# Kernel optimization log

Hardware: AMD Instinct MI355X
Metric: run time of the kernel (lower is better)

Reference implementation:

```python
import jax, jax.numpy as jnp
import numpy as np

B, C, H, W = 4, 64, 256, 256
P, PRIOR, HID, HEADS, NPROMPT = 4, 64, 128, 4, 4
TOKEN = C * P * P  # 1024
RATIO = 0.25


def _patchify(x):
    b, c, h, w = x.shape
    gh, gw = h // P, w // P
    t = x.reshape(b, c, gh, P, gw, P).transpose(0, 2, 4, 1, 3, 5).reshape(b, gh * gw, c * P * P)
    return t, (b, c, gh, gw)


def _unpatchify(t, meta):
    b, c, gh, gw = meta
    return t.reshape(b, gh, gw, c, P, P).transpose(0, 3, 1, 4, 2, 5).reshape(b, c, gh * P, gw * P)


def _coords(gh, gw):
    ys = (jnp.arange(gh, dtype=jnp.float32) + 0.5) / gh
    xs = (jnp.arange(gw, dtype=jnp.float32) + 0.5) / gw
    yy, xx = jnp.meshgrid(ys, xs, indexing='ij')
    return jnp.stack([yy.ravel(), xx.ravel()], axis=-1)  # [N, 2]


def setup_inputs():
    key = jax.random.key(0)
    ks = iter(jax.random.split(key, 32))
    rn = lambda *s: jax.random.normal(next(ks), s, jnp.float32)
    w = lambda *s: rn(*s) * 0.02
    z = lambda *s: jnp.zeros(s, jnp.float32)
    return dict(
        vis_feat=rn(B, C, H, W),
        ir_feat=rn(B, C, H, W),
        prompt_bank=w(NPROMPT, PRIOR),
        Wr=w(2 * C, NPROMPT), br=z(NPROMPT),
        br_Wtok=w(2, 2 * TOKEN, HID), br_Wpri=w(2, PRIOR, HID), br_Wco=w(2, 2, HID),
        br_bs=z(2, HID), br_Wout=w(2, HID), br_bout=z(2),
        br_Wq=w(2, TOKEN, HID), br_Wk=w(2, TOKEN, HID), br_Wv=w(2, TOKEN, HID),
        br_Wo=w(2, HID, TOKEN), br_Wint=w(2, PRIOR, HID),
        br_Wbyp=w(2, 2 * TOKEN, TOKEN), br_bbyp=z(2, TOKEN),
        conv1_w=w(C, C, 3, 3), conv1_b=z(C),
        conv2_w=w(C, C, 3, 3), conv2_b=z(C),
        Wa1=w(PRIOR, 2 * C), ba1=z(2 * C),
        Wa2=w(2 * C, 2 * C), ba2=z(2 * C),
    )


def reference(vis_feat, ir_feat, prompt_bank, Wr, br, br_Wtok, br_Wpri, br_Wco, br_bs, br_Wout, br_bout, br_Wq, br_Wk, br_Wv, br_Wo, br_Wint, br_Wbyp, br_bbyp, conv1_w, conv1_b, conv2_w, conv2_b, Wa1, ba1, Wa2, ba2):
    # intent router: pooled features -> prompt mixture -> intent vector
    pooled = jnp.concatenate([vis_feat.mean((2, 3)), ir_feat.mean((2, 3))], -1)  # [B, 2C]
    prompt_weight = jax.nn.softmax(pooled @ Wr + br, -1)  # [B, NPROMPT]
    intent = prompt_weight @ prompt_bank  # [B, PRIOR]

    def split(x):
        F = jnp.fft.fft2(x)
        return jnp.abs(F), jnp.angle(F)

    vamp, vph = split(vis_feat)
    iamp, iph = split(ir_feat)

    def fuse(vm, im, i):
        vt, meta = _patchify(vm)
        it_, _ = _patchify(im)
        b, c, gh, gw = meta
        n = gh * gw
        coords = _coords(gh, gw)
        # token score net: tokens + intent + coord embedding -> scalar score per token
        h = (jnp.concatenate([vt, it_], -1) @ br_Wtok[i]
             + (intent @ br_Wpri[i])[:, None, :]
             + (coords @ br_Wco[i])[None] + br_bs[i])
        score = jax.nn.gelu(h) @ br_Wout[i] + br_bout[i]  # [B, N]
        k = max(1, int(n * RATIO))
        topk_val, topk_idx = jax.lax.top_k(score, k)
        gth = lambda t: jnp.take_along_axis(t, topk_idx[:, :, None], axis=1)
        vs, irs = gth(vt), gth(it_)  # [B, k, TOKEN]
        # selected-token cross attention (vis queries, ir keys/values), intent-modulated
        dh = HID // HEADS
        hd = lambda x, Wm: (x @ Wm).reshape(b, k, HEADS, dh)
        q, kk, vv = hd(vs, br_Wq[i]), hd(irs, br_Wk[i]), hd(irs, br_Wv[i])
        attn = jax.nn.softmax(jnp.einsum('bqhd,bkhd->bhqk', q, kk) / jnp.float32(np.sqrt(dh)), -1)
        o = jnp.einsum('bhqk,bkhd->bqhd', attn, vv).reshape(b, k, HID)
        o = o + (intent @ br_Wint[i])[:, None, :]
        fused_sel = vs + o @ br_Wo[i]  # [B, k, TOKEN]
        # lightweight bypass on all tokens (gated blend), then scatter selected back
        g = jax.nn.sigmoid(jnp.concatenate([vt, it_], -1) @ br_Wbyp[i] + br_bbyp[i])
        full = g * vt + (1.0 - g) * it_
        full = full.at[jnp.arange(b)[:, None], topk_idx].set(fused_sel)
        return _unpatchify(full, meta)

    famp = fuse(vamp, iamp, 0)
    fph = fuse(vph, iph, 1)
    fph = jnp.arctan2(jnp.sin(fph), jnp.cos(fph))  # phase wrap to (-pi, pi]
    spec = jax.lax.complex(famp * jnp.cos(fph), famp * jnp.sin(fph))
    spatial = jnp.fft.ifft2(spec).real

    conv = lambda x, wgt, bia: jax.lax.conv_general_dilated(
        x, wgt, (1, 1), 'SAME', dimension_numbers=('NCHW', 'OIHW', 'NCHW')) + bia[None, :, None, None]
    y = conv(jax.nn.relu(conv(spatial, conv1_w, conv1_b)), conv2_w, conv2_b)
    aff = jax.nn.gelu(intent @ Wa1 + ba1) @ Wa2 + ba2  # [B, 2C]
    gamma, beta = aff[:, :C], aff[:, C:]
    y = y * (1.0 + 0.1 * jnp.tanh(gamma))[:, :, None, None] + 0.1 * beta[:, :, None, None]
    return y + 0.5 * (vis_feat + ir_feat)
```

## Files before the change

kernel.cpp:

```cpp
#include <hip/hip_runtime.h>

typedef unsigned int uint;
typedef unsigned short ushort;
typedef unsigned long long u64;
typedef __attribute__((ext_vector_type(8))) short short8;
typedef __attribute__((ext_vector_type(4))) float f32x4;

__device__ __forceinline__ uint brev8(uint x){ return __brev(x) >> 24; }
__device__ __forceinline__ float geluf(float x){
  return 0.5f*x*(1.f + tanhf(0.7978845608028654f*(x + 0.044715f*x*x*x)));
}
__device__ __forceinline__ ushort f2bf(float f){
  unsigned u = __float_as_uint(f);
  unsigned r = u + 0x7FFFu + ((u >> 16) & 1u);
  return (ushort)(r >> 16);
}
__device__ __forceinline__ float bf2f(ushort u){
  return __uint_as_float((uint)u << 16);
}

__global__ __launch_bounds__(256) void kern_pool(const float* __restrict__ vis,
                                                 const float* __restrict__ irf,
                                                 float* __restrict__ pooled){
  __shared__ float red[256];
  int bc = blockIdx.x;
  int b = bc >> 7, cc = bc & 127;
  const float* src = (cc < 64) ? (vis + (size_t)(b*64+cc)*65536)
                               : (irf + (size_t)(b*64+(cc-64))*65536);
  float s = 0.f;
  for (int i = threadIdx.x; i < 65536; i += 256) s += src[i];
  red[threadIdx.x] = s;
  __syncthreads();
  for (int off = 128; off > 0; off >>= 1){
    if (threadIdx.x < off) red[threadIdx.x] += red[threadIdx.x + off];
    __syncthreads();
  }
  if (threadIdx.x == 0) pooled[bc] = red[0] * (1.f/65536.f);
}

__global__ __launch_bounds__(256) void kern_small(const float* __restrict__ pooled,
    const float* __restrict__ Wr, const float* __restrict__ br,
    const float* __restrict__ bank, const float* __restrict__ Wpri,
    const float* __restrict__ Wint, const float* __restrict__ Wa1,
    const float* __restrict__ ba1, const float* __restrict__ Wa2,
    const float* __restrict__ ba2,
    float* __restrict__ IP, float* __restrict__ IPint,
    float* __restrict__ modg, float* __restrict__ modb){
  __shared__ float logit_s[16];
  __shared__ float pw_s[16];
  __shared__ float intent_s[4][64];
  __shared__ float t1_s[4][128];
  int t = threadIdx.x;
  if (t < 16){
    int b = t >> 2, j = t & 3;
    float s = br[j];
    for (int k = 0; k < 128; ++k) s += pooled[b*128+k]*Wr[k*4+j];
    logit_s[t] = s;
  }
  __syncthreads();
  if (t < 4){
    int b = t;
    float m = logit_s[b*4];
    for (int j = 1; j < 4; ++j) m = fmaxf(m, logit_s[b*4+j]);
    float e[4], sum = 0.f;
    for (int j = 0; j < 4; ++j){ e[j] = expf(logit_s[b*4+j]-m); sum += e[j]; }
    for (int j = 0; j < 4; ++j) pw_s[b*4+j] = e[j]/sum;
  }
  __syncthreads();
  {
    int b = t >> 6, p = t & 63;
    float s = 0.f;
    for (int j = 0; j < 4; ++j) s += pw_s[b*4+j]*bank[j*64+p];
    intent_s[b][p] = s;
  }
  __syncthreads();
  for (int o = t; o < 1024; o += 256){
    int i = o >> 9, rem = o & 511, b = rem >> 7, n = rem & 127;
    float s1 = 0.f, s2 = 0.f;
    for (int p = 0; p < 64; ++p){
      float iv = intent_s[b][p];
      s1 += iv * Wpri[(i*64+p)*128 + n];
      s2 += iv * Wint[(i*64+p)*128 + n];
    }
    IP[o] = s1; IPint[o] = s2;
  }
  for (int o = t; o < 512; o += 256){
    int b = o >> 7, n = o & 127;
    float s = ba1[n];
    for (int p = 0; p < 64; ++p) s += intent_s[b][p]*Wa1[p*128+n];
    t1_s[b][n] = geluf(s);
  }
  __syncthreads();
  for (int o = t; o < 512; o += 256){
    int b = o >> 7, n = o & 127;
    float s = ba2[n];
    for (int p = 0; p < 128; ++p) s += t1_s[b][p]*Wa2[p*128+n];
    if (n < 64) modg[b*64+n] = 1.f + 0.1f*tanhf(s);
    else        modb[b*64+(n-64)] = 0.1f*s;
  }
}

__global__ __launch_bounds__(256) void kern_fft_rows_fwd(const float* __restrict__ x,
    float* __restrict__ sre, float* __restrict__ sim){
  __shared__ float re[2][256], im[2][256];
  __shared__ float twr[128], twi[128];
  int t = threadIdx.x;
  if (t < 128){
    float a = -6.2831853071795864f * (float)t * (1.f/256.f);
    sincosf(a, &twi[t], &twr[t]);
  }
  int r = t >> 7, jj = t & 127;
  size_t row = (size_t)blockIdx.x*2 + r;
  {
    const float* xp = x + row*256;
    re[r][jj] = xp[jj]; re[r][jj+128] = xp[jj+128];
    im[r][jj] = 0.f;    im[r][jj+128] = 0.f;
  }
  __syncthreads();
  for (int s = 0; s < 8; ++s){
    int half = 128 >> s;
    int j = jj & (half-1);
    int g = jj >> (7-s);
    int k = (g << (8-s)) + j;
    int m = j << s;
    float wc = twr[m], ws = twi[m];
    float are = re[r][k],      aim = im[r][k];
    float bre = re[r][k+half], bim = im[r][k+half];
    re[r][k] = are + bre; im[r][k] = aim + bim;
    float tr = are - bre, ti = aim - bim;
    re[r][k+half] = tr*wc - ti*ws;
    im[r][k+half] = tr*ws + ti*wc;
    __syncthreads();
  }
  {
    float* orp = sre + row*256; float* oip = sim + row*256;
    int w1 = jj, w2 = jj + 128;
    orp[w1] = re[r][brev8(w1)]; oip[w1] = im[r][brev8(w1)];
    orp[w2] = re[r][brev8(w2)]; oip[w2] = im[r][brev8(w2)];
  }
}

__global__ __launch_bounds__(256) void kern_ifft_rows_spec(const float* __restrict__ famp,
    const float* __restrict__ fph, float* __restrict__ sre, float* __restrict__ sim){
  __shared__ float re[4][256], im[4][256];
  __shared__ float twr[128], twi[128];
  int t = threadIdx.x;
  if (t < 128){
    float a = -6.2831853071795864f * (float)t * (1.f/256.f);
    sincosf(a, &twi[t], &twr[t]);
  }
  int R = blockIdx.x * 4;
  {
    int r = t >> 6, q = t & 63;
    int row = R + r;
    int bc = row >> 8, h = row & 255;
    int b = bc >> 6, c = bc & 63;
    size_t addr = ((size_t)(b*4096 + (h>>2)*64 + q))*1024 + c*16 + (h&3)*4;
    float4 a4 = *(const float4*)(famp + addr);
    float4 p4 = *(const float4*)(fph + addr);
    float sn, cs;
    sincosf(p4.x, &sn, &cs); re[r][4*q+0] = a4.x*cs; im[r][4*q+0] = a4.x*sn;
    sincosf(p4.y, &sn, &cs); re[r][4*q+1] = a4.y*cs; im[r][4*q+1] = a4.y*sn;
    sincosf(p4.z, &sn, &cs); re[r][4*q+2] = a4.z*cs; im[r][4*q+2] = a4.z*sn;
    sincosf(p4.w, &sn, &cs); re[r][4*q+3] = a4.w*cs; im[r][4*q+3] = a4.w*sn;
  }
  __syncthreads();
  for (int s = 0; s < 8; ++s){
    int half = 128 >> s;
    #pragma unroll
    for (int bi0 = 0; bi0 < 2; ++bi0){
      int bi = t + bi0*256;
      int r = bi >> 7, tj = bi & 127;
      int j = tj & (half-1);
      int g = tj >> (7-s);
      int k = (g << (8-s)) + j;
      int m = j << s;
      float wc = twr[m], ws = -twi[m];
      float are = re[r][k],      aim = im[r][k];
      float bre = re[r][k+half], bim = im[r][k+half];
      re[r][k] = are + bre; im[r][k] = aim + bim;
      float tr = are - bre, ti = aim - bim;
      re[r][k+half] = tr*wc - ti*ws;
      im[r][k+half] = tr*ws + ti*wc;
    }
    __syncthreads();
  }
  {
    int r = t >> 6, q = t & 63;
    size_t row = (size_t)R + r;
    float4 vr, vi;
    vr.x = re[r][brev8(4*q+0)]; vi.x = im[r][brev8(4*q+0)];
    vr.y = re[r][brev8(4*q+1)]; vi.y = im[r][brev8(4*q+1)];
    vr.z = re[r][brev8(4*q+2)]; vi.z = im[r][brev8(4*q+2)];
    vr.w = re[r][brev8(4*q+3)]; vi.w = im[r][brev8(4*q+3)];
    *(float4*)(sre + row*256 + 4*q) = vr;
    *(float4*)(sim + row*256 + 4*q) = vi;
  }
}

template<int DIR>
__global__ __launch_bounds__(256) void kern_fft_cols(const float* __restrict__ sre,
    const float* __restrict__ sim, void* __restrict__ out0, void* __restrict__ out1){
  __shared__ float reL[256*17];
  __shared__ float imL[256*17];
  __shared__ float twr[128], twi[128];
  int t = threadIdx.x;
  if (t < 128){
    float a = -6.2831853071795864f * (float)t * (1.f/256.f);
    sincosf(a, &twi[t], &twr[t]);
  }
  int img = blockIdx.x >> 4;
  int c0 = (blockIdx.x & 15) * 16;
  {
    const float* pr = sre + ((size_t)img*256 + t)*256 + c0;
    const float* pi = sim + ((size_t)img*256 + t)*256 + c0;
    #pragma unroll
    for (int p = 0; p < 4; ++p){
      float4 vr = *(const float4*)(pr + 4*p);
      float4 vi = *(const float4*)(pi + 4*p);
      int base = t*17 + 4*p;
      reL[base+0]=vr.x; reL[base+1]=vr.y; reL[base+2]=vr.z; reL[base+3]=vr.w;
      imL[base+0]=vi.x; imL[base+1]=vi.y; imL[base+2]=vi.z; imL[base+3]=vi.w;
    }
  }
  __syncthreads();
  int col = t & 15, tb = t >> 4;
  for (int s = 0; s < 8; ++s){
    int half = 128 >> s;
    #pragma unroll
    for (int it = 0; it < 8; ++it){
      int tj = tb + it*16;
      int j = tj & (half-1);
      int g = tj >> (7-s);
      int k = (g << (8-s)) + j;
      int m = j << s;
      float wc = twr[m];
      float ws = (DIR == 0) ? twi[m] : -twi[m];
      int i0 = k*17 + col, i1 = (k+half)*17 + col;
      float are = reL[i0], aim = imL[i0];
      float bre = reL[i1], bim = imL[i1];
      reL[i0] = are + bre; imL[i0] = aim + bim;
      float tr = are - bre, ti = aim - bim;
      reL[i1] = tr*wc - ti*ws;
      imL[i1] = tr*ws + ti*wc;
    }
    __syncthreads();
  }
  int b = img >> 6, c = img & 63;
  int h = t; int src = (int)brev8((uint)h);
  if (DIR == 0){
    ushort* oa = (ushort*)out0;
    ushort* op = (ushort*)out1;
    int gy = h >> 2, py = h & 3;
    #pragma unroll
    for (int p = 0; p < 4; ++p){
      int base = src*17 + 4*p;
      float a0, a1, a2, a3, p0, p1, p2, p3;
      float rr, ii;
      rr = reL[base+0]; ii = imL[base+0]; a0 = sqrtf(rr*rr+ii*ii); p0 = atan2f(ii, rr);
      rr = reL[base+1]; ii = imL[base+1]; a1 = sqrtf(rr*rr+ii*ii); p1 = atan2f(ii, rr);
      rr = reL[base+2]; ii = imL[base+2]; a2 = sqrtf(rr*rr+ii*ii); p2 = atan2f(ii, rr);
      rr = reL[base+3]; ii = imL[base+3]; a3 = sqrtf(rr*rr+ii*ii); p3 = atan2f(ii, rr);
      size_t addr = ((size_t)(b*4096 + gy*64 + (c0>>2) + p))*1024 + c*16 + py*4;
      uint2 av, pv;
      av.x = (uint)f2bf(a0) | ((uint)f2bf(a1) << 16);
      av.y = (uint)f2bf(a2) | ((uint)f2bf(a3) << 16);
      pv.x = (uint)f2bf(p0) | ((uint)f2bf(p1) << 16);
      pv.y = (uint)f2bf(p2) | ((uint)f2bf(p3) << 16);
      *(uint2*)(oa + addr) = av;
      *(uint2*)(op + addr) = pv;
    }
  } else {
    float* op = (float*)out0 + ((size_t)img*256 + h)*256 + c0;
    #pragma unroll
    for (int p = 0; p < 4; ++p){
      int base = src*17 + 4*p;
      float4 v;
      v.x = reL[base+0]*(1.f/65536.f);
      v.y = reL[base+1]*(1.f/65536.f);
      v.z = reL[base+2]*(1.f/65536.f);
      v.w = reL[base+3]*(1.f/65536.f);
      *(float4*)(op + 4*p) = v;
    }
  }
}

struct TRS {
  const float* src[10];
  ushort* dst[10];
  int K[10], N[10];
  int start[11];
};
__global__ __launch_bounds__(256) void kern_tr(TRS p){
  __shared__ float lds[32][33];
  int bid = blockIdx.x;
  int e = 0;
  while (bid >= p.start[e+1]) ++e;
  int tloc = bid - p.start[e];
  int tilesN = p.N[e] >> 5;
  int tn = tloc % tilesN, tk = tloc / tilesN;
  int k0 = tk << 5, n0 = tn << 5;
  const float* src = p.src[e];
  ushort* dst = p.dst[e];
  int K = p.K[e], N = p.N[e];
  int r = threadIdx.x >> 5, c = threadIdx.x & 31;
  #pragma unroll
  for (int i = 0; i < 4; ++i)
    lds[r + 8*i][c] = src[(size_t)(k0 + r + 8*i)*N + n0 + c];
  __syncthreads();
  #pragma unroll
  for (int i = 0; i < 4; ++i)
    dst[(size_t)(n0 + r + 8*i)*K + k0 + c] = f2bf(lds[c][r + 8*i]);
}

struct GP2 {
  const ushort* A0[6];
  const ushort* Bt[6];
  float* Cm[6];
  const int* idxp[6];
  int N, K;
};

__global__ __launch_bounds__(256) void kern_mgemm2(GP2 p){
  __shared__ __align__(16) ushort Asb[64*64];
  __shared__ __align__(16) ushort Bsb[128*64];
  __shared__ int idx_s[64];
  int z = blockIdx.z;
  const ushort* A0 = p.A0[z];
  const ushort* Bt = p.Bt[z];
  float* Cm = p.Cm[z];
  int tid = threadIdx.x;
  int m0 = blockIdx.x * 64;
  int n0 = blockIdx.y * 128;
  int lane = tid & 63, w = tid >> 6;
  int wr = w & 1, wc = w >> 1;
  int lr = lane & 15, ql = lane >> 4;

  if (tid < 64){
    int m = m0 + tid;
    idx_s[tid] = p.idxp[z][(m >> 10)*1024 + (m & 1023)];
  }
  __syncthreads();
  int gb = m0 >> 10;

  f32x4 acc[2][4];
  #pragma unroll
  for (int i = 0; i < 2; ++i)
    #pragma unroll
    for (int j = 0; j < 4; ++j) acc[i][j] = (f32x4){0.f,0.f,0.f,0.f};

  int kh = tid & 7;
  int rA = tid >> 3;
  for (int k0 = 0; k0 < p.K; k0 += 64){
    #pragma unroll
    for (int s = 0; s < 2; ++s){
      int m = rA + 32*s;
      const ushort* ap = A0 + ((size_t)(gb << 12) + idx_s[m])*(size_t)p.K + k0 + kh*8;
      short8 v = *(const short8*)ap;
      int byte = m*128 + ((kh*16) ^ ((m & 7)*16));
      *(short8*)((char*)Asb + byte) = v;
    }
    #pragma unroll
    for (int s = 0; s < 4; ++s){
      int n = rA + 32*s;
      short8 v = *(const short8*)(Bt + (size_t)(n0+n)*p.K + k0 + kh*8);
      int byte = n*128 + ((kh*16) ^ ((n & 7)*16));
      *(short8*)((char*)Bsb + byte) = v;
    }
    __syncthreads();
    short8 af[2][2], bf[4][2];
    #pragma unroll
    for (int fm = 0; fm < 2; ++fm){
      int row = wr*32 + fm*16 + lr;
      #pragma unroll
      for (int kq = 0; kq < 2; ++kq){
        int byte = row*128 + ((kq*64 + ql*16) ^ ((row & 7)*16));
        af[fm][kq] = *(const short8*)((const char*)Asb + byte);
      }
    }
    #pragma unroll
    for (int fn = 0; fn < 4; ++fn){
      int row = wc*64 + fn*16 + lr;
      #pragma unroll
      for (int kq = 0; kq < 2; ++kq){
        int byte = row*128 + ((kq*64 + ql*16) ^ ((row & 7)*16));
        bf[fn][kq] = *(const short8*)((const char*)Bsb + byte);
      }
    }
    #pragma unroll
    for (int kq = 0; kq < 2; ++kq)
      #pragma unroll
      for (int fm = 0; fm < 2; ++fm)
        #pragma unroll
        for (int fn = 0; fn < 4; ++fn)
          acc[fm][fn] = __builtin_amdgcn_mfma_f32_16x16x32_bf16(af[fm][kq], bf[fn][kq],
                                                                acc[fm][fn], 0, 0, 0);
    __syncthreads();
  }

  #pragma unroll
  for (int fm = 0; fm < 2; ++fm){
    #pragma unroll
    for (int fn = 0; fn < 4; ++fn){
      int n = n0 + wc*64 + fn*16 + lr;
      #pragma unroll
      for (int reg = 0; reg < 4; ++reg){
        int m = m0 + wr*32 + fm*16 + ql*4 + reg;
        Cm[(size_t)m*p.N + n] = acc[fm][fn][reg];
      }
    }
  }
}

struct GP3 {
  const ushort* A0[2];
  const ushort* A1[2];
  const ushort* Bt[2];
  float* Ch[2];
  float* Cm[2];
  const float* ep0[2];
  const float* ep1[2];
  const float* ep2[2];
  const float* bias[2];
  const ushort* vt[2];
  const ushort* it[2];
  int K;
};

__global__ __launch_bounds__(256) void kern_mgemm3(GP3 p){
  __shared__ __align__(16) ushort Asb[128*64];
  __shared__ __align__(16) ushort Bsb[128*64];
  int z = blockIdx.z;
  const ushort* Bt = p.Bt[z];
  int tid = threadIdx.x;
  int m0 = blockIdx.x * 128;
  int n0 = blockIdx.y * 128;
  int lane = tid & 63, w = tid >> 6;
  int wr = w & 1, wc = w >> 1;
  int lr = lane & 15, ql = lane >> 4;

  f32x4 acc[4][4];
  #pragma unroll
  for (int i = 0; i < 4; ++i)
    #pragma unroll
    for (int j = 0; j < 4; ++j) acc[i][j] = (f32x4){0.f,0.f,0.f,0.f};

  int kh = tid & 7;
  int rA = tid >> 3;
  for (int k0 = 0; k0 < p.K; k0 += 64){
    const ushort* Asrc = (k0 < 1024) ? p.A0[z] : p.A1[z];
    int kk = (k0 & 1023) + kh*8;
    #pragma unroll
    for (int s = 0; s < 4; ++s){
      int m = rA + 32*s;
      short8 v = *(const short8*)(Asrc + (size_t)(m0+m)*1024 + kk);
      int byte = m*128 + ((kh*16) ^ ((m & 7)*16));
      *(short8*)((char*)Asb + byte) = v;
    }
    #pragma unroll
    for (int s = 0; s < 4; ++s){
      int n = rA + 32*s;
      short8 v = *(const short8*)(Bt + (size_t)(n0+n)*p.K + k0 + kh*8);
      int byte = n*128 + ((kh*16) ^ ((n & 7)*16));
      *(short8*)((char*)Bsb + byte) = v;
    }
    __syncthreads();
    short8 af[4][2], bf[4][2];
    #pragma unroll
    for (int fm = 0; fm < 4; ++fm){
      int row = wr*64 + fm*16 + lr;
      #pragma unroll
      for (int kq = 0; kq < 2; ++kq){
        int byte = row*128 + ((kq*64 + ql*16) ^ ((row & 7)*16));
        af[fm][kq] = *(const short8*)((const char*)Asb + byte);
      }
    }
    #pragma unroll
    for (int fn = 0; fn < 4; ++fn){
      int row = wc*64 + fn*16 + lr;
      #pragma unroll
      for (int kq = 0; kq < 2; ++kq){
        int byte = row*128 + ((kq*64 + ql*16) ^ ((row & 7)*16));
        bf[fn][kq] = *(const short8*)((const char*)Bsb + byte);
      }
    }
    #pragma unroll
    for (int kq = 0; kq < 2; ++kq)
      #pragma unroll
      for (int fm = 0; fm < 4; ++fm)
        #pragma unroll
        for (int fn = 0; fn < 4; ++fn)
          acc[fm][fn] = __builtin_amdgcn_mfma_f32_16x16x32_bf16(af[fm][kq], bf[fn][kq],
                                                                acc[fm][fn], 0, 0, 0);
    __syncthreads();
  }

  if (blockIdx.y == 0){
    float* Ch = p.Ch[z];
    #pragma unroll
    for (int fm = 0; fm < 4; ++fm){
      #pragma unroll
      for (int fn = 0; fn < 4; ++fn){
        int n = wc*64 + fn*16 + lr;
        #pragma unroll
        for (int reg = 0; reg < 4; ++reg){
          int m = m0 + wr*64 + fm*16 + ql*4 + reg;
          int bl = m >> 12, g = m & 4095;
          int gy = g >> 6, gx = g & 63;
          float cy = ((float)gy + 0.5f)*(1.f/64.f);
          float cx = ((float)gx + 0.5f)*(1.f/64.f);
          float o = acc[fm][fn][reg] + p.ep0[z][bl*128 + n] + cy*p.ep1[z][n]
                  + cx*p.ep1[z][128 + n] + p.ep2[z][n];
          Ch[(size_t)m*128 + n] = o;
        }
      }
    }
  } else {
    float* Cm = p.Cm[z];
    const ushort* vtp = p.vt[z];
    const ushort* itp = p.it[z];
    int nb = n0 - 128;
    #pragma unroll
    for (int fm = 0; fm < 4; ++fm){
      #pragma unroll
      for (int fn = 0; fn < 4; ++fn){
        int n = nb + wc*64 + fn*16 + lr;
        float bia = p.bias[z][n];
        #pragma unroll
        for (int reg = 0; reg < 4; ++reg){
          int m = m0 + wr*64 + fm*16 + ql*4 + reg;
          size_t off = (size_t)m*1024 + n;
          float vt = bf2f(vtp[off]);
          float it = bf2f(itp[off]);
          float gg = 1.f/(1.f + expf(-(acc[fm][fn][reg] + bia)));
          Cm[off] = gg*vt + (1.f-gg)*it;
        }
      }
    }
  }
}

struct SCP {
  const float* A0[2];
  const float* Bm[2];
  float* Cm[2];
  const int* idxp[2];
  const ushort* vtb[2];
};

__global__ __launch_bounds__(256) void kern_scat(SCP p){
  __shared__ __align__(16) ushort Asb[64*40];
  __shared__ __align__(16) ushort Bsb[128*40];
  __shared__ int idx_s[64];
  int z = blockIdx.z;
  const float* A0 = p.A0[z];
  const float* Bm = p.Bm[z];
  float* Cm = p.Cm[z];
  int tid = threadIdx.x;
  int m0 = blockIdx.y * 64;
  int n0 = blockIdx.x * 128;
  int lane = tid & 63, w = tid >> 6;
  int wr = w & 1, wc = w >> 1;
  int lr = lane & 15, ql = lane >> 4;
  if (tid < 64){
    int m = m0 + tid;
    idx_s[tid] = p.idxp[z][(m >> 10)*1024 + (m & 1023)];
  }
  __syncthreads();
  int gb = m0 >> 10;

  f32x4 acc[2][4];
  #pragma unroll
  for (int i = 0; i < 2; ++i)
    #pragma unroll
    for (int j = 0; j < 4; ++j) acc[i][j] = (f32x4){0.f,0.f,0.f,0.f};

  for (int k0 = 0; k0 < 128; k0 += 32){
    {
      int m = tid & 63;
      int khh = (tid >> 6) * 8;
      const float* ap = A0 + (size_t)(m0+m)*128 + k0 + khh;
      float4 f0 = *(const float4*)ap;
      float4 f1 = *(const float4*)(ap + 4);
      short8 v;
      v[0]=(short)f2bf(f0.x); v[1]=(short)f2bf(f0.y);
      v[2]=(short)f2bf(f0.z); v[3]=(short)f2bf(f0.w);
      v[4]=(short)f2bf(f1.x); v[5]=(short)f2bf(f1.y);
      v[6]=(short)f2bf(f1.z); v[7]=(short)f2bf(f1.w);
      *(short8*)&Asb[m*40 + khh] = v;
    }
    #pragma unroll
    for (int e0 = 0; e0 < 512; e0 += 256){
      int e = e0 + tid;
      int n = e & 127;
      int khh = (e >> 7) * 8;
      const float* bp = Bm + (size_t)(k0+khh)*1024 + n0 + n;
      short8 v;
      #pragma unroll
      for (int j = 0; j < 8; ++j) v[j] = (short)f2bf(bp[(size_t)j*1024]);
      *(short8*)&Bsb[n*40 + khh] = v;
    }
    __syncthreads();
    short8 af[2], bf[4];
    #pragma unroll
    for (int fr = 0; fr < 2; ++fr)
      af[fr] = *(const short8*)&Asb[(wr*32 + fr*16 + lr)*40 + ql*8];
    #pragma unroll
    for (int fc = 0; fc < 4; ++fc)
      bf[fc] = *(const short8*)&Bsb[(wc*64 + fc*16 + lr)*40 + ql*8];
    #pragma unroll
    for (int fr = 0; fr < 2; ++fr)
      #pragma unroll
      for (int fc = 0; fc < 4; ++fc)
        acc[fr][fc] = __builtin_amdgcn_mfma_f32_16x16x32_bf16(af[fr], bf[fc],
                                                              acc[fr][fc], 0, 0, 0);
    __syncthreads();
  }

  #pragma unroll
  for (int fr = 0; fr < 2; ++fr){
    #pragma unroll
    for (int fc = 0; fc < 4; ++fc){
      int n = n0 + wc*64 + fc*16 + lr;
      #pragma unroll
      for (int reg = 0; reg < 4; ++reg){
        int mloc = wr*32 + fr*16 + ql*4 + reg;
        int gt = idx_s[mloc];
        size_t off = ((size_t)(gb << 12) + gt)*1024 + n;
        Cm[off] = acc[fr][fc][reg] + bf2f(p.vtb[z][off]);
      }
    }
  }
}

__global__ __launch_bounds__(64) void kern_score(const float* __restrict__ h,
    const float* __restrict__ wout, const float* __restrict__ bout,
    float* __restrict__ score, int Mper){
  int m = blockIdx.x, br = blockIdx.y, t = threadIdx.x;
  const float* hp = h + ((size_t)br*Mper + m)*128;
  const float* wp = wout + br*128;
  float s = geluf(hp[t])*wp[t] + geluf(hp[t+64])*wp[t+64];
  #pragma unroll
  for (int off = 32; off > 0; off >>= 1) s += __shfl_down(s, off);
  if (t == 0) score[(size_t)br*Mper + m] = s + bout[br];
}

__global__ __launch_bounds__(1024) void kern_topk(const float* __restrict__ score,
    int* __restrict__ idx_out){
  __shared__ u64 keys[4096];
  int b = blockIdx.x, t = threadIdx.x;
  for (int i = t; i < 4096; i += 1024){
    float s = score[b*4096 + i];
    uint u = __float_as_uint(s);
    uint msk = (u & 0x80000000u) ? ~u : (u | 0x80000000u);
    keys[i] = ((u64)msk << 32) | (uint)(4095 - i);
  }
  __syncthreads();
  for (int k = 2; k <= 4096; k <<= 1){
    for (int j = k >> 1; j > 0; j >>= 1){
      for (int i = t; i < 4096; i += 1024){
        int l = i ^ j;
        if (l > i){
          u64 a = keys[i], c = keys[l];
          bool descB = ((i & k) == 0);
          bool sw = descB ? (a < c) : (a > c);
          if (sw){ keys[i] = c; keys[l] = a; }
        }
      }
      __syncthreads();
    }
  }
  idx_out[b*1024 + t] = 4095 - (int)(keys[t] & 0xFFFFFFFFu);
}

__global__ __launch_bounds__(128) void kern_attn_part(const float* __restrict__ qb,
    const float* __restrict__ kb, const float* __restrict__ vb,
    float* __restrict__ paoa, float* __restrict__ pml){
  __shared__ float Ks[64][32];
  __shared__ float Vs[64][32];
  int t = threadIdx.x;
  int hh = blockIdx.y;
  int zc = blockIdx.z;
  int zf = zc >> 2, c = zc & 3;
  size_t boff = (size_t)zf*131072;
  int jq = blockIdx.x*128 + t;
  float qv[32];
  {
    const float4* qp = (const float4*)(qb + boff + (size_t)jq*128 + hh*32);
    #pragma unroll
    for (int d = 0; d < 8; ++d) ((float4*)qv)[d] = qp[d];
  }
  float mrun = -3.0e38f, lrun = 0.f;
  float oa[32];
  #pragma unroll
  for (int d = 0; d < 32; ++d) oa[d] = 0.f;
  for (int kt = 0; kt < 4; ++kt){
    int k0 = c*256 + kt*64;
    #pragma unroll
    for (int rep = 0; rep < 4; ++rep){
      int f = t + rep*128;
      int r = f >> 3, q4 = f & 7;
      size_t base = boff + (size_t)(k0 + r)*128 + hh*32 + 4*q4;
      *(float4*)&Ks[r][4*q4] = *(const float4*)(kb + base);
      *(float4*)&Vs[r][4*q4] = *(const float4*)(vb + base);
    }
    __syncthreads();
    #pragma unroll
    for (int st = 0; st < 4; ++st){
      float s[16];
      #pragma unroll
      for (int j = 0; j < 16; ++j){
        float v = 0.f;
        #pragma unroll
        for (int d = 0; d < 32; ++d) v += qv[d]*Ks[st*16+j][d];
        s[j] = v * 0.17677669529663687f;
      }
      float mt = s[0];
      #pragma unroll
      for (int j = 1; j < 16; ++j) mt = fmaxf(mt, s[j]);
      float mnew = fmaxf(mrun, mt);
      float alpha = expf(mrun - mnew);
      lrun *= alpha;
      #pragma unroll
      for (int d = 0; d < 32; ++d) oa[d] *= alpha;
      #pragma unroll
      for (int j = 0; j < 16; ++j){
        float pe = expf(s[j] - mnew);
        lrun += pe;
        #pragma unroll
        for (int d = 0; d < 32; ++d) oa[d] += pe*Vs[st*16+j][d];
      }
      mrun = mnew;
    }
    __syncthreads();
  }
  size_t rec = (((size_t)zf*4 + hh)*4 + c)*1024 + jq;
  float* pp = paoa + rec*32;
  #pragma unroll
  for (int d = 0; d < 8; ++d) ((float4*)pp)[d] = ((float4*)oa)[d];
  pml[rec*2]   = mrun;
  pml[rec*2+1] = lrun;
}

__global__ __launch_bounds__(256) void kern_attn_comb(const float* __restrict__ paoa,
    const float* __restrict__ pml, float* __restrict__ ob,
    const float* __restrict__ ipint, int PB, int b0){
  int t = threadIdx.x;
  int hh = blockIdx.y, zf = blockIdx.z;
  int jq = blockIdx.x*256 + t;
  size_t rbase = (((size_t)zf*4 + hh)*4)*1024 + jq;
  float mc[4], lc[4];
  #pragma unroll
  for (int c = 0; c < 4; ++c){
    mc[c] = pml[(rbase + c*1024)*2];
    lc[c] = pml[(rbase + c*1024)*2 + 1];
  }
  float M = fmaxf(fmaxf(mc[0], mc[1]), fmaxf(mc[2], mc[3]));
  float wgt[4], L = 0.f;
  #pragma unroll
  for (int c = 0; c < 4; ++c){ wgt[c] = expf(mc[c] - M); L += lc[c]*wgt[c]; }
  float inv = 1.f/L;
  int br = (zf >= PB) ? 1 : 0;
  int bb = zf - br*PB;
  const float* ip = ipint + br*512 + (b0+bb)*128 + hh*32;
  float* op = ob + (size_t)zf*131072 + (size_t)jq*128 + hh*32;
  #pragma unroll
  for (int d = 0; d < 32; ++d){
    float o = 0.f;
    #pragma unroll
    for (int c = 0; c < 4; ++c) o += paoa[(rbase + c*1024)*32 + d]*wgt[c];
    op[d] = o*inv + ip[d];
  }
}

__global__ __launch_bounds__(256) void kern_wt(const float* __restrict__ w1,
    const float* __restrict__ w2, ushort* __restrict__ wt){
  int blk = blockIdx.x;
  const float* src = (blk < 9) ? w1 : w2;
  int tap = blk - (blk < 9 ? 0 : 9);
  ushort* dst = wt + (blk < 9 ? 0 : 36864) + tap*4096;
  for (int e = threadIdx.x; e < 4096; e += 256){
    dst[e] = f2bf(src[(size_t)e*9 + tap]);
  }
}

template<int MODE>
__global__ __launch_bounds__(256) void kern_cmfma(const float* __restrict__ in,
    const ushort* __restrict__ wt, const float* __restrict__ bias,
    float* __restrict__ out,
    const float* __restrict__ modg, const float* __restrict__ modb,
    const float* __restrict__ vis, const float* __restrict__ irf){
  __shared__ __align__(16) ushort ins[64][268];
  int t = threadIdx.x;
  int y = blockIdx.x, b = blockIdx.y;
  int lane = t & 63, w = t >> 6;
  int wc = w & 1, wx = w >> 1;
  int lr = lane & 15, ql = lane >> 4;

  f32x4 acc[2][8];
  #pragma unroll
  for (int f = 0; f < 2; ++f)
    #pragma unroll
    for (int xf = 0; xf < 8; ++xf) acc[f][xf] = (f32x4){0.f,0.f,0.f,0.f};

  for (int dy = 0; dy < 3; ++dy){
    int yy = y + dy - 1;
    if (yy < 0 || yy > 255) continue;
    const float* src = in + ((size_t)(b*64)*256 + yy)*256;
    #pragma unroll
    for (int s = 0; s < 16; ++s){
      int e = t + s*256;
      int ci = e >> 6, q = e & 63;
      float4 f4 = *(const float4*)(src + (size_t)ci*65536 + 4*q);
      uint lo = (uint)f2bf(f4.x) | ((uint)f2bf(f4.y) << 16);
      uint hi = (uint)f2bf(f4.z) | ((uint)f2bf(f4.w) << 16);
      *(uint2*)&ins[ci][4*q + 4] = make_uint2(lo, hi);
    }
    if (t < 128){
      int r = t & 63;
      ins[r][(t >> 6) ? 260 : 3] = 0;
    }
    __syncthreads();
    short8 wf[2][3][2];
    #pragma unroll
    for (int kk = 0; kk < 2; ++kk)
      #pragma unroll
      for (int dx = 0; dx < 3; ++dx)
        #pragma unroll
        for (int f = 0; f < 2; ++f)
          wf[kk][dx][f] = *(const short8*)(wt +
            (size_t)((dy*3 + dx)*64 + 32*wc + 16*f + lr)*64 + kk*32 + ql*8);
    #pragma unroll
    for (int kk = 0; kk < 2; ++kk){
      const ushort* bp = &ins[kk*32 + ql*8][0];
      #pragma unroll
      for (int dx = 0; dx < 3; ++dx){
        int xb = 128*wx + lr + dx + 3;
        #pragma unroll
        for (int xf = 0; xf < 8; ++xf){
          int xi = xb + 16*xf;
          short8 bf;
          #pragma unroll
          for (int e = 0; e < 8; ++e) bf[e] = (short)bp[e*268 + xi];
          acc[0][xf] = __builtin_amdgcn_mfma_f32_16x16x32_bf16(wf[kk][dx][0], bf,
                                                               acc[0][xf], 0, 0, 0);
          acc[1][xf] = __builtin_amdgcn_mfma_f32_16x16x32_bf16(wf[kk][dx][1], bf,
                                                               acc[1][xf], 0, 0, 0);
        }
      }
    }
    __syncthreads();
  }

  #pragma unroll
  for (int f = 0; f < 2; ++f){
    #pragma unroll
    for (int xf = 0; xf < 8; ++xf){
      int x = 128*wx + 16*xf + lr;
      #pragma unroll
      for (int reg = 0; reg < 4; ++reg){
        int co = 32*wc + 16*f + ql*4 + reg;
        float v = acc[f][xf][reg] + bias[co];
        size_t oi = ((size_t)(b*64 + co)*256 + y)*256 + x;
        if (MODE == 1){
          out[oi] = fmaxf(v, 0.f);
        } else {
          out[oi] = v*modg[b*64+co] + modb[b*64+co] + 0.5f*(vis[oi] + irf[oi]);
        }
      }
    }
  }
}

extern "C" void kernel_launch(void* const* d_in, const int* in_sizes, int n_in,
                              void* d_out, int out_size, void* d_ws, size_t ws_size,
                              hipStream_t stream){
  (void)in_sizes; (void)n_in; (void)out_size;
  const float* vis  = (const float*)d_in[0];
  const float* irf  = (const float*)d_in[1];
  const float* bank = (const float*)d_in[2];
  const float* Wr   = (const float*)d_in[3];
  const float* br   = (const float*)d_in[4];
  const float* Wtok = (const float*)d_in[5];
  const float* Wpri = (const float*)d_in[6];
  const float* Wco  = (const float*)d_in[7];
  const float* bs   = (const float*)d_in[8];
  const float* Wout = (const float*)d_in[9];
  const float* bout = (const float*)d_in[10];
  const float* Wq   = (const float*)d_in[11];
  const float* Wk   = (const float*)d_in[12];
  const float* Wv   = (const float*)d_in[13];
  const float* Wo   = (const float*)d_in[14];
  const float* Wint = (const float*)d_in[15];
  const float* Wbyp = (const float*)d_in[16];
  const float* bbyp = (const float*)d_in[17];
  const float* c1w  = (const float*)d_in[18];
  const float* c1b  = (const float*)d_in[19];
  const float* c2w  = (const float*)d_in[20];
  const float* c2b  = (const float*)d_in[21];
  const float* Wa1  = (const float*)d_in[22];
  const float* ba1  = (const float*)d_in[23];
  const float* Wa2  = (const float*)d_in[24];
  const float* ba2  = (const float*)d_in[25];

  auto needB = [](int PB)->size_t{
    return ((size_t)PB*14755840 + 2792448) * 4;
  };
  const int PB = (ws_size >= needB(4)) ? 4 : (ws_size >= needB(2)) ? 2 : 1;

  float* ws = (float*)d_ws;
  const size_t PLF = (size_t)PB*4194304;
  float* PH4 = ws;
  ushort* ABV = (ushort*)(ws + PLF);
  ushort* PBV = ABV + PLF;
  ushort* ABI = PBV + PLF;
  ushort* PBI = ABI + PLF;
  float* S0 = ws + PLF;
  float* S1 = S0 + PLF;
  float* sm = ws + 3*PLF;
  float* hbuf  = sm; sm += (size_t)2*PB*524288;
  float* qbuf  = sm; sm += (size_t)2*PB*131072;
  float* kbuf  = sm; sm += (size_t)2*PB*131072;
  float* vbuf  = sm; sm += (size_t)2*PB*131072;
  float* obuf  = sm; sm += (size_t)2*PB*131072;
  float* score = sm; sm += (size_t)2*PB*4096;
  int*   idxb  = (int*)sm; sm += (size_t)2*PB*1024;
  float* pml   = sm; sm += (size_t)PB*65536;
  ushort* BTcomb = (ushort*)sm;
  ushort* BTq    = BTcomb + 4718592;
  ushort* BTk    = BTq + 262144;
  ushort* BTv    = BTk + 262144;
  sm += 2752512;
  float* pooled= sm; sm += 512;
  float* IP    = sm; sm += 1024;
  float* IPint = sm; sm += 1024;
  float* modg  = sm; sm += 256;
  float* modb  = sm; sm += 256;
  ushort* wtb = (ushort*)sm; sm += 36864;
  float* paoa = hbuf;

  kern_pool <<<512, 256, 0, stream>>>(vis, irf, pooled);
  kern_small<<<1, 256, 0, stream>>>(pooled, Wr, br, bank, Wpri, Wint,
                                    Wa1, ba1, Wa2, ba2, IP, IPint, modg, modb);
  kern_wt   <<<18, 256, 0, stream>>>(c1w, c2w, wtb);
  {
    TRS tr{};
    const float* srcs[10] = {Wtok, Wtok+262144, Wbyp, Wbyp+2097152,
                             Wq, Wq+131072, Wk, Wk+131072, Wv, Wv+131072};
    ushort* dsts[10] = {BTcomb, BTcomb+2359296, BTcomb+262144, BTcomb+2359296+262144,
                        BTq, BTq+131072, BTk, BTk+131072, BTv, BTv+131072};
    int Ks[10] = {2048,2048,2048,2048,1024,1024,1024,1024,1024,1024};
    int Ns[10] = {128,128,1024,1024,128,128,128,128,128,128};
    int tiles[10] = {256,256,2048,2048,128,128,128,128,128,128};
    int acc0 = 0;
    for (int i = 0; i < 10; ++i){
      tr.src[i] = srcs[i]; tr.dst[i] = dsts[i];
      tr.K[i] = Ks[i]; tr.N[i] = Ns[i];
      tr.start[i] = acc0; acc0 += tiles[i];
    }
    tr.start[10] = acc0;
    kern_tr<<<acc0, 256, 0, stream>>>(tr);
  }

  for (int b0 = 0; b0 < 4; b0 += PB){
    const float* vis_b = vis + (size_t)b0*4194304;
    const float* ir_b  = irf + (size_t)b0*4194304;
    float* OUT = (float*)d_out + (size_t)b0*4194304;

    kern_fft_rows_fwd<<<PB*8192, 256, 0, stream>>>(vis_b, OUT, PH4);
    kern_fft_cols<0> <<<PB*1024, 256, 0, stream>>>(OUT, PH4, ABV, PBV);
    kern_fft_rows_fwd<<<PB*8192, 256, 0, stream>>>(ir_b, OUT, PH4);
    kern_fft_cols<0> <<<PB*1024, 256, 0, stream>>>(OUT, PH4, ABI, PBI);

    {
      GP3 p{};
      p.A0[0]=ABV; p.A1[0]=ABI; p.A0[1]=PBV; p.A1[1]=PBI;
      p.vt[0]=ABV; p.it[0]=ABI; p.vt[1]=PBV; p.it[1]=PBI;
      p.Cm[0]=OUT; p.Cm[1]=PH4;
      for (int z = 0; z < 2; ++z){
        p.Bt[z] = BTcomb + (size_t)z*2359296;
        p.Ch[z] = hbuf + (size_t)z*PB*524288;
        p.ep0[z] = IP + z*512 + b0*128;
        p.ep1[z] = Wco + z*256;
        p.ep2[z] = bs + z*128;
        p.bias[z] = bbyp + z*1024;
      }
      p.K = 2048;
      kern_mgemm3<<<dim3(PB*32, 9, 2), 256, 0, stream>>>(p);
    }
    kern_score<<<dim3(PB*4096, 2), 64, 0, stream>>>(hbuf, Wout, bout, score, PB*4096);
    kern_topk <<<2*PB, 1024, 0, stream>>>(score, idxb);
    {
      GP2 p{};
      const ushort* Aplanes[6] = {ABV, ABI, ABI, PBV, PBI, PBI};
      const ushort* Bmats[6] = {BTq, BTk, BTv, BTq+131072, BTk+131072, BTv+131072};
      float* Cms[6] = {qbuf, kbuf, vbuf,
                       qbuf+(size_t)PB*131072, kbuf+(size_t)PB*131072,
                       vbuf+(size_t)PB*131072};
      for (int z = 0; z < 6; ++z){
        p.A0[z] = Aplanes[z]; p.Bt[z] = Bmats[z]; p.Cm[z] = Cms[z];
        p.idxp[z] = idxb + (z < 3 ? 0 : PB*1024);
      }
      p.N = 128; p.K = 1024;
      kern_mgemm2<<<dim3(PB*16, 1, 6), 256, 0, stream>>>(p);
    }
    kern_attn_part<<<dim3(8, 4, 2*PB*4), 128, 0, stream>>>(qbuf, kbuf, vbuf,
                                                           paoa, pml);
    kern_attn_comb<<<dim3(4, 4, 2*PB), 256, 0, stream>>>(paoa, pml, obuf,
                                                         IPint, PB, b0);
    {
      SCP p{};
      p.A0[0]=obuf; p.A0[1]=obuf+(size_t)PB*131072;
      p.Bm[0]=Wo; p.Bm[1]=Wo+131072;
      p.Cm[0]=OUT; p.Cm[1]=PH4;
      p.vtb[0]=ABV; p.vtb[1]=PBV;
      p.idxp[0]=idxb; p.idxp[1]=idxb+PB*1024;
      kern_scat<<<dim3(8, PB*16, 2), 256, 0, stream>>>(p);
    }

    kern_ifft_rows_spec<<<PB*4096, 256, 0, stream>>>(OUT, PH4, S0, S1);
    kern_fft_cols<1>   <<<PB*1024, 256, 0, stream>>>(S0, S1, OUT, nullptr);
  }

  kern_cmfma<1><<<dim3(256, 4), 256, 0, stream>>>((float*)d_out, wtb, c1b, ws,
                                                  nullptr, nullptr, nullptr, nullptr);
  kern_cmfma<2><<<dim3(256, 4), 256, 0, stream>>>(ws, wtb + 36864, c2b, (float*)d_out,
                                                  modg, modb, vis, irf);
}
```

Before: 1.411 ms.

## Fuse score GEMV into hidden GEMM and compute bypass only for unselected tokens

Splits the combined token-hidden plus bypass GEMM into two kernels. The hidden-projection kernel now applies GELU and the output projection in its epilogue and writes scores directly, which removes the hidden-buffer round trip and the separate score kernel. After top-k, a new kernel builds the list of unselected token indices. The bypass GEMM then runs only over those 3072 of 4096 tokens per batch, using gathered A rows, since the selected rows are overwritten later anyway. This saves about a quarter of the bypass FLOPs but adds a kernel launch and serializes the bypass behind top-k.

```diff
diff --git a/kernel.cpp b/kernel.cpp
--- a/kernel.cpp
+++ b/kernel.cpp
@@ -412,29 +412,27 @@
   }
 }
 
-struct GP3 {
+struct HSP {
   const ushort* A0[2];
   const ushort* A1[2];
   const ushort* Bt[2];
-  float* Ch[2];
-  float* Cm[2];
+  float* score;
   const float* ep0[2];
   const float* ep1[2];
   const float* ep2[2];
-  const float* bias[2];
-  const ushort* vt[2];
-  const ushort* it[2];
-  int K;
+  const float* wout;
+  const float* bout;
+  int Mper;
 };
 
-__global__ __launch_bounds__(256) void kern_mgemm3(GP3 p){
+__global__ __launch_bounds__(256) void kern_hscore(HSP p){
   __shared__ __align__(16) ushort Asb[128*64];
   __shared__ __align__(16) ushort Bsb[128*64];
+  __shared__ float part[2][128];
   int z = blockIdx.z;
   const ushort* Bt = p.Bt[z];
   int tid = threadIdx.x;
   int m0 = blockIdx.x * 128;
-  int n0 = blockIdx.y * 128;
   int lane = tid & 63, w = tid >> 6;
   int wr = w & 1, wc = w >> 1;
   int lr = lane & 15, ql = lane >> 4;
@@ -447,7 +445,7 @@
 
   int kh = tid & 7;
   int rA = tid >> 3;
-  for (int k0 = 0; k0 < p.K; k0 += 64){
+  for (int k0 = 0; k0 < 2048; k0 += 64){
     const ushort* Asrc = (k0 < 1024) ? p.A0[z] : p.A1[z];
     int kk = (k0 & 1023) + kh*8;
     #pragma unroll
@@ -460,7 +458,7 @@
     #pragma unroll
     for (int s = 0; s < 4; ++s){
       int n = rA + 32*s;
-      short8 v = *(const short8*)(Bt + (size_t)(n0+n)*p.K + k0 + kh*8);
+      short8 v = *(const short8*)(Bt + (size_t)n*2048 + k0 + kh*8);
       int byte = n*128 + ((kh*16) ^ ((n & 7)*16));
       *(short8*)((char*)Bsb + byte) = v;
     }
@@ -495,46 +493,157 @@
     __syncthreads();
   }
 
-  if (blockIdx.y == 0){
-    float* Ch = p.Ch[z];
-    #pragma unroll
-    for (int fm = 0; fm < 4; ++fm){
+  float wv[4];
+  #pragma unroll
+  for (int fn = 0; fn < 4; ++fn) wv[fn] = p.wout[z*128 + wc*64 + fn*16 + lr];
+  #pragma unroll
+  for (int fm = 0; fm < 4; ++fm){
+    #pragma unroll
+    for (int reg = 0; reg < 4; ++reg){
+      int m = m0 + wr*64 + fm*16 + ql*4 + reg;
+      int bl = m >> 12, g = m & 4095;
+      int gy = g >> 6, gx = g & 63;
+      float cy = ((float)gy + 0.5f)*(1.f/64.f);
+      float cx = ((float)gx + 0.5f)*(1.f/64.f);
+      float ps = 0.f;
       #pragma unroll
       for (int fn = 0; fn < 4; ++fn){
         int n = wc*64 + fn*16 + lr;
+        float o = acc[fm][fn][reg] + p.ep0[z][bl*128 + n] + cy*p.ep1[z][n]
+                + cx*p.ep1[z][128 + n] + p.ep2[z][n];
+        ps += geluf(o)*wv[fn];
+      }
+      #pragma unroll
+      for (int off = 8; off > 0; off >>= 1) ps += __shfl_xor(ps, off);
+      if (lr == 0) part[wc][wr*64 + fm*16 + ql*4 + reg] = ps;
+    }
+  }
+  __syncthreads();
+  if (tid < 128)
+    p.score[(size_t)z*p.Mper + m0 + tid] = part[0][tid] + part[1][tid] + p.bout[z];
+}
+
+__global__ __launch_bounds__(1024) void kern_nsel(const int* __restrict__ idxb,
+    int* __restrict__ nsel){
+  __shared__ unsigned char mask[4096];
+  __shared__ int cnt;
+  int b = blockIdx.x, t = threadIdx.x;
+  *(uint*)&mask[4*t] = 0;
+  if (t == 0) cnt = 0;
+  __syncthreads();
+  mask[idxb[b*1024 + t]] = 1;
+  __syncthreads();
+  for (int i = t; i < 4096; i += 1024){
+    if (!mask[i]){
+      int pos = atomicAdd(&cnt, 1);
+      nsel[(size_t)b*3072 + pos] = i;
+    }
+  }
+}
+
+struct BYP {
+  const ushort* A0[2];
+  const ushort* A1[2];
+  const ushort* Bt[2];
+  float* Cm[2];
+  const int* nsel[2];
+  const float* bias[2];
+  const ushort* vt[2];
+  const ushort* it[2];
+};
+
+__global__ __launch_bounds__(256) void kern_byp(BYP p){
+  __shared__ __align__(16) ushort Asb[128*64];
+  __shared__ __align__(16) ushort Bsb[128*64];
+  __shared__ int idx_s[128];
+  int z = blockIdx.z;
+  const ushort* Bt = p.Bt[z];
+  int tid = threadIdx.x;
+  int gb  = blockIdx.x / 24;
+  int m0l = (blockIdx.x % 24) * 128;
+  int n0 = blockIdx.y * 128;
+  int lane = tid & 63, w = tid >> 6;
+  int wr = w & 1, wc = w >> 1;
+  int lr = lane & 15, ql = lane >> 4;
+
+  if (tid < 128)
+    idx_s[tid] = p.nsel[z][(size_t)gb*3072 + m0l + tid];
+  __syncthreads();
+
+  f32x4 acc[4][4];
+  #pragma unroll
+  for (int i = 0; i < 4; ++i)
+    #pragma unroll
+    for (int j = 0; j < 4; ++j) acc[i][j] = (f32x4){0.f,0.f,0.f,0.f};
+
+  int kh = tid & 7;
+  int rA = tid >> 3;
+  for (int k0 = 0; k0 < 2048; k0 += 64){
+    const ushort* Asrc = (k0 < 1024) ? p.A0[z] : p.A1[z];
+    int kk = (k0 & 1023) + kh*8;
+    #pragma unroll
+    for (int s = 0; s < 4; ++s){
+      int m = rA + 32*s;
+      size_t grow = (size_t)(gb << 12) + idx_s[m];
+      short8 v = *(const short8*)(Asrc + grow*1024 + kk);
+      int byte = m*128 + ((kh*16) ^ ((m & 7)*16));
+      *(short8*)((char*)Asb + byte) = v;
+    }
+    #pragma unroll
+    for (int s = 0; s < 4; ++s){
+      int n = rA + 32*s;
+      short8 v = *(const short8*)(Bt + (size_t)(n0+n)*2048 + k0 + kh*8);
+      int byte = n*128 + ((kh*16) ^ ((n & 7)*16));
+      *(short8*)((char*)Bsb + byte) = v;
+    }
+    __syncthreads();
+    short8 af[4][2], bf[4][2];
+    #pragma unroll
+    for (int fm = 0; fm < 4; ++fm){
+      int row = wr*64 + fm*16 + lr;
+      #pragma unroll
+      for (int kq = 0; kq < 2; ++kq){
+        int byte = row*128 + ((kq*64 + ql*16) ^ ((row & 7)*16));
+        af[fm][kq] = *(const short8*)((const char*)Asb + byte);
+      }
+    }
+    #pragma unroll
+    for (int fn = 0; fn < 4; ++fn){
+      int row = wc*64 + fn*16 + lr;
+      #pragma unroll
+      for (int kq = 0; kq < 2; ++kq){
+        int byte = row*128 + ((kq*64 + ql*16) ^ ((row & 7)*16));
+        bf[fn][kq] = *(const short8*)((const char*)Bsb + byte);
+      }
+    }
+    #pragma unroll
+    for (int kq = 0; kq < 2; ++kq)
+      #pragma unroll
+      for (int fm = 0; fm < 4; ++fm)
         #pragma unroll
-        for (int reg = 0; reg < 4; ++reg){
-          int m = m0 + wr*64 + fm*16 + ql*4 + reg;
-          int bl = m >> 12, g = m & 4095;
-          int gy = g >> 6, gx = g & 63;
-          float cy = ((float)gy + 0.5f)*(1.f/64.f);
-          float cx = ((float)gx + 0.5f)*(1.f/64.f);
-          float o = acc[fm][fn][reg] + p.ep0[z][bl*128 + n] + cy*p.ep1[z][n]
-                  + cx*p.ep1[z][128 + n] + p.ep2[z][n];
-          Ch[(size_t)m*128 + n] = o;
-        }
-      }
-    }
-  } else {
-    float* Cm = p.Cm[z];
-    const ushort* vtp = p.vt[z];
-    const ushort* itp = p.it[z];
-    int nb = n0 - 128;
-    #pragma unroll
-    for (int fm = 0; fm < 4; ++fm){
-      #pragma unroll
-      for (int fn = 0; fn < 4; ++fn){
-        int n = nb + wc*64 + fn*16 + lr;
-        float bia = p.bias[z][n];
-        #pragma unroll
-        for (int reg = 0; reg < 4; ++reg){
-          int m = m0 + wr*64 + fm*16 + ql*4 + reg;
-          size_t off = (size_t)m*1024 + n;
-          float vt = bf2f(vtp[off]);
-          float it = bf2f(itp[off]);
-          float gg = 1.f/(1.f + expf(-(acc[fm][fn][reg] + bia)));
-          Cm[off] = gg*vt + (1.f-gg)*it;
-        }
+        for (int fn = 0; fn < 4; ++fn)
+          acc[fm][fn] = __builtin_amdgcn_mfma_f32_16x16x32_bf16(af[fm][kq], bf[fn][kq],
+                                                                acc[fm][fn], 0, 0, 0);
+    __syncthreads();
+  }
+
+  float* Cm = p.Cm[z];
+  const ushort* vtp = p.vt[z];
+  const ushort* itp = p.it[z];
+  #pragma unroll
+  for (int fm = 0; fm < 4; ++fm){
+    #pragma unroll
+    for (int fn = 0; fn < 4; ++fn){
+      int n = n0 + wc*64 + fn*16 + lr;
+      float bia = p.bias[z][n];
+      #pragma unroll
+      for (int reg = 0; reg < 4; ++reg){
+        int mloc = wr*64 + fm*16 + ql*4 + reg;
+        size_t off = ((size_t)(gb << 12) + idx_s[mloc])*1024 + n;
+        float vt = bf2f(vtp[off]);
+        float it = bf2f(itp[off]);
+        float gg = 1.f/(1.f + expf(-(acc[fm][fn][reg] + bia)));
+        Cm[off] = gg*vt + (1.f-gg)*it;
       }
     }
   }
@@ -631,18 +740,6 @@
       }
     }
   }
-}
-
-__global__ __launch_bounds__(64) void kern_score(const float* __restrict__ h,
-    const float* __restrict__ wout, const float* __restrict__ bout,
-    float* __restrict__ score, int Mper){
-  int m = blockIdx.x, br = blockIdx.y, t = threadIdx.x;
-  const float* hp = h + ((size_t)br*Mper + m)*128;
-  const float* wp = wout + br*128;
-  float s = geluf(hp[t])*wp[t] + geluf(hp[t+64])*wp[t+64];
-  #pragma unroll
-  for (int off = 32; off > 0; off >>= 1) s += __shfl_down(s, off);
-  if (t == 0) score[(size_t)br*Mper + m] = s + bout[br];
 }
 
 __global__ __launch_bounds__(1024) void kern_topk(const float* __restrict__ score,
@@ -926,10 +1023,11 @@
   float* score = sm; sm += (size_t)2*PB*4096;
   int*   idxb  = (int*)sm; sm += (size_t)2*PB*1024;
   float* pml   = sm; sm += (size_t)PB*65536;
-  ushort* BTcomb = (ushort*)sm;
-  ushort* BTq    = BTcomb + 4718592;
-  ushort* BTk    = BTq + 262144;
-  ushort* BTv    = BTk + 262144;
+  ushort* BTtok = (ushort*)sm;
+  ushort* BTbyp = BTtok + 524288;
+  ushort* BTq   = BTbyp + 4194304;
+  ushort* BTk   = BTq + 262144;
+  ushort* BTv   = BTk + 262144;
   sm += 2752512;
   float* pooled= sm; sm += 512;
   float* IP    = sm; sm += 1024;
@@ -937,7 +1035,8 @@
   float* modg  = sm; sm += 256;
   float* modb  = sm; sm += 256;
   ushort* wtb = (ushort*)sm; sm += 36864;
-  float* paoa = hbuf;
+  int*   nselb = (int*)hbuf;
+  float* paoa  = hbuf;
 
   kern_pool <<<512, 256, 0, stream>>>(vis, irf, pooled);
   kern_small<<<1, 256, 0, stream>>>(pooled, Wr, br, bank, Wpri, Wint,
@@ -947,7 +1046,7 @@
     TRS tr{};
     const float* srcs[10] = {Wtok, Wtok+262144, Wbyp, Wbyp+2097152,
                              Wq, Wq+131072, Wk, Wk+131072, Wv, Wv+131072};
-    ushort* dsts[10] = {BTcomb, BTcomb+2359296, BTcomb+262144, BTcomb+2359296+262144,
+    ushort* dsts[10] = {BTtok, BTtok+262144, BTbyp, BTbyp+2097152,
                         BTq, BTq+131072, BTk, BTk+131072, BTv, BTv+131072};
     int Ks[10] = {2048,2048,2048,2048,1024,1024,1024,1024,1024,1024};
     int Ns[10] = {128,128,1024,1024,128,128,128,128,128,128};
@@ -973,23 +1072,32 @@
     kern_fft_cols<0> <<<PB*1024, 256, 0, stream>>>(OUT, PH4, ABI, PBI);
 
     {
-      GP3 p{};
+      HSP p{};
+      p.A0[0]=ABV; p.A1[0]=ABI; p.A0[1]=PBV; p.A1[1]=PBI;
+      for (int z = 0; z < 2; ++z){
+        p.Bt[z] = BTtok + (size_t)z*262144;
+        p.ep0[z] = IP + z*512 + b0*128;
+        p.ep1[z] = Wco + z*256;
+        p.ep2[z] = bs + z*128;
+      }
+      p.score = score; p.wout = Wout; p.bout = bout;
+      p.Mper = PB*4096;
+      kern_hscore<<<dim3(PB*32, 1, 2), 256, 0, stream>>>(p);
+    }
+    kern_topk<<<2*PB, 1024, 0, stream>>>(score, idxb);
+    kern_nsel<<<2*PB, 1024, 0, stream>>>(idxb, nselb);
+    {
+      BYP p{};
       p.A0[0]=ABV; p.A1[0]=ABI; p.A0[1]=PBV; p.A1[1]=PBI;
       p.vt[0]=ABV; p.it[0]=ABI; p.vt[1]=PBV; p.it[1]=PBI;
       p.Cm[0]=OUT; p.Cm[1]=PH4;
       for (int z = 0; z < 2; ++z){
-        p.Bt[z] = BTcomb + (size_t)z*2359296;
-        p.Ch[z] = hbuf + (size_t)z*PB*524288;
-        p.ep0[z] = IP + z*512 + b0*128;
-        p.ep1[z] = Wco + z*256;
-        p.ep2[z] = bs + z*128;
+        p.Bt[z] = BTbyp + (size_t)z*2097152;
         p.bias[z] = bbyp + z*1024;
-      }
-      p.K = 2048;
-      kern_mgemm3<<<dim3(PB*32, 9, 2), 256, 0, stream>>>(p);
-    }
-    kern_score<<<dim3(PB*4096, 2), 64, 0, stream>>>(hbuf, Wout, bout, score, PB*4096);
-    kern_topk <<<2*PB, 1024, 0, stream>>>(score, idxb);
+        p.nsel[z] = nselb + (size_t)z*PB*3072;
+      }
+      kern_byp<<<dim3(PB*24, 8, 2), 256, 0, stream>>>(p);
+    }
     {
       GP2 p{};
       const ushort* Aplanes[6] = {ABV, ABI, ABI, PBV, PBI, PBI};
```

After: 1.365 ms. 1.03x faster.
